# Optimization experiments

Measured on AMD Instinct MI355X. Metric: run time of the kernel, lower is better.

## Reference

```python
import jax, jax.numpy as jnp
import numpy as np

N = 100000   # nodes
E = 3200000  # edges (before self-loops)
H = 16       # hidden_dim
G = 1000     # graphs in batch
NEG_SLOPE = 0.2


def setup_inputs() -> dict:
    key = jax.random.key(0)
    ks = jax.random.split(key, 40)
    rn = lambda k, s: (jax.random.normal(k, s, jnp.float32) * 0.1)
    inp = {}
    inp['x'] = jax.random.normal(ks[0], (N, 1), jnp.float32)
    inp['edge_index'] = jax.random.randint(ks[1], (2, E), 0, N, jnp.int64)
    inp['batch'] = jnp.sort(jax.random.randint(ks[2], (N,), 0, G, jnp.int64))
    dims = [1, H, H]
    i = 3
    for l in range(3):
        d = dims[l]
        inp[f'c{l}_Wl'] = rn(ks[i], (d, H)); i += 1
        inp[f'c{l}_bl'] = jnp.zeros((H,), jnp.float32)
        inp[f'c{l}_Wr'] = rn(ks[i], (d, H)); i += 1
        inp[f'c{l}_br'] = jnp.zeros((H,), jnp.float32)
        inp[f'c{l}_att'] = rn(ks[i], (H,)); i += 1
        inp[f'c{l}_bias'] = jnp.zeros((H,), jnp.float32)
        inp[f'l{l}_W'] = rn(ks[i], (H, H)); i += 1
        inp[f'l{l}_b'] = jnp.zeros((H,), jnp.float32)
    for j, (a, b) in enumerate([(H, H), (H, H), (H, 1)]):
        inp[f'o{j}_W'] = rn(ks[i], (a, b)); i += 1
        inp[f'o{j}_b'] = jnp.zeros((b,), jnp.float32)
    return inp


def gatv2_conv(x, src, dst, Wl, bl, Wr, br, att, bias):
    # PyG GATv2Conv, heads=1: x_j = lin_l(x)[src], x_i = lin_r(x)[dst]
    xl = x @ Wl + bl  # [N,H] source transform
    xr = x @ Wr + br  # [N,H] target transform
    e = jax.nn.leaky_relu(xl[src] + xr[dst], NEG_SLOPE)  # [E+N,H]
    score = e @ att  # [E+N]
    # scatter-softmax over incoming edges of each destination node
    m = jax.ops.segment_max(score, dst, num_segments=N)
    ex = jnp.exp(score - m[dst])
    denom = jax.ops.segment_sum(ex, dst, num_segments=N)
    alpha = ex / denom[dst]
    out = jax.ops.segment_sum(alpha[:, None] * xl[src], dst, num_segments=N)
    return out + bias


def reference(x, c0_Wl, c0_bl, c0_Wr, c0_br, c0_att, c0_bias,
              c1_Wl, c1_bl, c1_Wr, c1_br, c1_att, c1_bias,
              c2_Wl, c2_bl, c2_Wr, c2_br, c2_att, c2_bias,
              l0_W, l0_b, l1_W, l1_b, l2_W, l2_b,
              o0_W, o0_b, o1_W, o1_b, o2_W, o2_b,
              edge_index, batch):
    # add self-loops (PyG GATv2Conv default add_self_loops=True)
    loops = jnp.arange(N, dtype=edge_index.dtype)
    ei = jnp.concatenate([edge_index, jnp.stack([loops, loops])], axis=1)
    src, dst = ei[0], ei[1]
    convs = [(c0_Wl, c0_bl, c0_Wr, c0_br, c0_att, c0_bias),
             (c1_Wl, c1_bl, c1_Wr, c1_br, c1_att, c1_bias),
             (c2_Wl, c2_bl, c2_Wr, c2_br, c2_att, c2_bias)]
    lins = [(l0_W, l0_b), (l1_W, l1_b), (l2_W, l2_b)]
    h = x
    for (Wl, bl, Wr, br, att, bias), (W, b) in zip(convs, lins):
        h = jax.nn.relu(gatv2_conv(h, src, dst, Wl, bl, Wr, br, att, bias))
        h = h @ W + b
    g = jax.ops.segment_sum(h, batch, num_segments=G)  # global_add_pool -> [G,H]
    g = jax.nn.relu(g @ o0_W + o0_b)
    g = jax.nn.relu(g @ o1_W + o1_b)
    return g @ o2_W + o2_b  # [G,1]
```

## Files before the change

### kernel.cpp

```cpp
#include <hip/hip_runtime.h>
#include <hip/hip_fp16.h>

#define HD 16

static constexpr int NN = 100000;
static constexpr int EE = 3200000;
static constexpr int GG = 1000;
static constexpr int ET = EE + NN;
static constexpr float NEG = 0.2f;
static constexpr float LOG2E = 1.44269504f;

static constexpr int BSH = 8;
static constexpr int NB = (NN + 255) >> BSH;
static constexpr int EPB = 8192;
static constexpr int GB = (ET + EPB - 1) / EPB;
static constexpr int ITER = EPB / 1024;

__device__ __forceinline__ int imin(int a, int b) { return a < b ? a : b; }

__device__ __forceinline__ float h2f(unsigned short u) {
  __half_raw r; r.x = u;
  return __half2float((__half)r);
}

__device__ __forceinline__ float quad_sum(float v) {
  int a = __builtin_amdgcn_update_dpp(0, __float_as_int(v), 0xB1, 0xF, 0xF, true);
  v += __int_as_float(a);
  int b = __builtin_amdgcn_update_dpp(0, __float_as_int(v), 0x4E, 0xF, 0xF, true);
  return v + __int_as_float(b);
}

__global__ void k_chist(const int* __restrict__ edst, int* __restrict__ chist) {
  __shared__ int sh[NB];
  int t = threadIdx.x;
  for (int i = t; i < NB; i += 1024) sh[i] = 0;
  __syncthreads();
  int b0 = blockIdx.x * EPB;
#pragma unroll
  for (int i = 0; i < ITER; ++i) {
    int e = b0 + t + i * 1024;
    if (e < ET) {
      int d = (e < EE) ? edst[e] : e - EE;
      atomicAdd(&sh[d >> BSH], 1);
    }
  }
  __syncthreads();
  for (int i = t; i < NB; i += 1024)
    if (sh[i]) atomicAdd(&chist[i], sh[i]);
}

__global__ void k_cscan(const int* __restrict__ chist, int* __restrict__ cbase,
                        int* __restrict__ ccur, int* __restrict__ rowptr) {
  __shared__ int sh[512];
  int t = threadIdx.x;
  sh[t] = (t < NB) ? chist[t] : 0;
  __syncthreads();
  for (int off = 1; off < 512; off <<= 1) {
    int v = sh[t];
    int a = (t >= off) ? sh[t - off] : 0;
    __syncthreads();
    sh[t] = v + a;
    __syncthreads();
  }
  if (t < NB) {
    int b = (t == 0) ? 0 : sh[t - 1];
    cbase[t] = b;
    ccur[t] = b;
  }
  if (t == 0) rowptr[NN] = ET;
}

__global__ void k_csplit(const int* __restrict__ esrc, const int* __restrict__ edst,
                         int* __restrict__ ccur, unsigned* __restrict__ tmp) {
  __shared__ int hist[NB];
  __shared__ int base[NB];
  int t = threadIdx.x;
  for (int i = t; i < NB; i += 1024) hist[i] = 0;
  __syncthreads();
  int b0 = blockIdx.x * EPB;
  int sl[ITER], dl[ITER];
#pragma unroll
  for (int i = 0; i < ITER; ++i) {
    int e = b0 + t + i * 1024;
    int s = -1, d = 0;
    if (e < ET) {
      if (e < EE) { s = esrc[e]; d = edst[e]; } else { s = e - EE; d = s; }
      atomicAdd(&hist[d >> BSH], 1);
    }
    sl[i] = s; dl[i] = d;
  }
  __syncthreads();
  for (int i = t; i < NB; i += 1024) {
    int c = hist[i];
    base[i] = c ? atomicAdd(&ccur[i], c) : 0;
    hist[i] = 0;
  }
  __syncthreads();
#pragma unroll
  for (int i = 0; i < ITER; ++i) {
    int s = sl[i];
    if (s >= 0) {
      int d = dl[i], bb = d >> BSH;
      int slot = base[bb] + atomicAdd(&hist[bb], 1);
      tmp[slot] = ((unsigned)(d & 255) << 17) | (unsigned)s;
    }
  }
}

__global__ void k_fsort(const unsigned* __restrict__ tmp, const int* __restrict__ cbase,
                        const int* __restrict__ chist, int* __restrict__ rowptr,
                        int* __restrict__ psrc) {
  __shared__ int fh[256];
  __shared__ int fs[256];
  int b = blockIdx.x, t = threadIdx.x;
  if (t < 256) fh[t] = 0;
  __syncthreads();
  int beg = cbase[b], cnt = chist[b];
  for (int i = t; i < cnt; i += 1024)
    atomicAdd(&fh[tmp[beg + i] >> 17], 1);
  __syncthreads();
  if (t < 256) fs[t] = fh[t];
  __syncthreads();
  for (int off = 1; off < 256; off <<= 1) {
    int v = 0, a = 0;
    if (t < 256) { v = fs[t]; if (t >= off) a = fs[t - off]; }
    __syncthreads();
    if (t < 256) fs[t] = v + a;
    __syncthreads();
  }
  if (t < 256) {
    int ex = fs[t] - fh[t];
    fs[t] = ex;
    int node = (b << BSH) + t;
    if (node < NN) rowptr[node] = beg + ex;
  }
  __syncthreads();
  for (int i = t; i < cnt; i += 1024) {
    unsigned v = tmp[beg + i];
    int ld = v >> 17;
    psrc[beg + atomicAdd(&fs[ld], 1)] = (int)(v & 0x1FFFFu);
  }
}

__global__ void k_comb(const float* __restrict__ W0, const float* __restrict__ b0,
                       const float* __restrict__ Wl1, const float* __restrict__ bl1,
                       const float* __restrict__ Wr1, const float* __restrict__ br1,
                       const float* __restrict__ W1, const float* __restrict__ b1,
                       const float* __restrict__ Wl2, const float* __restrict__ bl2,
                       const float* __restrict__ Wr2, const float* __restrict__ br2,
                       float* __restrict__ Wc0l, float* __restrict__ bc0l,
                       float* __restrict__ Wc0r, float* __restrict__ bc0r,
                       float* __restrict__ Wc1l, float* __restrict__ bc1l,
                       float* __restrict__ Wc1r, float* __restrict__ bc1r) {
  const float *W, *b, *P, *bp;
  float *Wo, *bo;
  switch (blockIdx.x) {
    case 0:  W = W0; b = b0; P = Wl1; bp = bl1; Wo = Wc0l; bo = bc0l; break;
    case 1:  W = W0; b = b0; P = Wr1; bp = br1; Wo = Wc0r; bo = bc0r; break;
    case 2:  W = W1; b = b1; P = Wl2; bp = bl2; Wo = Wc1l; bo = bc1l; break;
    default: W = W1; b = b1; P = Wr2; bp = br2; Wo = Wc1r; bo = bc1r; break;
  }
  int t = threadIdx.x;
  int c = t >> 4, k = t & 15;
  float s = 0.f;
#pragma unroll
  for (int i = 0; i < 16; ++i) s = fmaf(W[c * 16 + i], P[i * 16 + k], s);
  Wo[t] = s;
  if (t < 16) {
    float sb = bp[t];
#pragma unroll
    for (int i = 0; i < 16; ++i) sb = fmaf(b[i], P[i * 16 + t], sb);
    bo[t] = sb;
  }
}

template <int MODE>
__global__ void k_conv(const int* __restrict__ rowptr, const int* __restrict__ psrc,
                       const float* __restrict__ x,
                       const float* __restrict__ Wl0, const float* __restrict__ bl0,
                       const float* __restrict__ Wr0, const float* __restrict__ br0,
                       const __half* __restrict__ xlh, const float* __restrict__ xr,
                       const float* __restrict__ att, const float* __restrict__ cbias,
                       const float* __restrict__ Wcl, const float* __restrict__ bcl,
                       const float* __restrict__ Wcr, const float* __restrict__ bcr,
                       const float* __restrict__ Wlast, const float* __restrict__ blast,
                       __half* __restrict__ oxlh, float* __restrict__ oxr,
                       float* __restrict__ gpool, const int* __restrict__ batch) {
  __shared__ float hsh[4][16];
  int gt = blockIdx.x * blockDim.x + threadIdx.x;
  int n = gt >> 6;
  if (n >= NN) return;
  int lane = threadIdx.x & 63;
  int q = lane & 3;
  int ei = lane >> 2;
  int k0 = q * 4;
  float4 att4 = *reinterpret_cast<const float4*>(att + k0);
  att4.x *= LOG2E; att4.y *= LOG2E; att4.z *= LOG2E; att4.w *= LOG2E;
  float4 xr4, wl4, bl4;
  if constexpr (MODE == 0) {
    wl4 = *reinterpret_cast<const float4*>(Wl0 + k0);
    bl4 = *reinterpret_cast<const float4*>(bl0 + k0);
    float4 wr4 = *reinterpret_cast<const float4*>(Wr0 + k0);
    float4 br4 = *reinterpret_cast<const float4*>(br0 + k0);
    float xn = x[n];
    xr4.x = fmaf(xn, wr4.x, br4.x);
    xr4.y = fmaf(xn, wr4.y, br4.y);
    xr4.z = fmaf(xn, wr4.z, br4.z);
    xr4.w = fmaf(xn, wr4.w, br4.w);
  } else {
    xr4 = *reinterpret_cast<const float4*>(xr + (size_t)n * HD + k0);
  }
  int beg = rowptr[n], end = rowptr[n + 1];
  int e1 = end - 1;
  int p = beg + ei;
  int s0 = psrc[imin(p, e1)];
  int s1 = psrc[imin(p + 16, e1)];
  float l0 = 0.f, l1 = 0.f;
  float a00 = 0.f, a01 = 0.f, a02 = 0.f, a03 = 0.f;
  float a10 = 0.f, a11 = 0.f, a12 = 0.f, a13 = 0.f;
  for (; p < end; p += 32) {
    int t0 = psrc[imin(p + 32, e1)];
    int t1 = psrc[imin(p + 48, e1)];
    float x00, x01, x02, x03, x10, x11, x12, x13;
    if constexpr (MODE == 0) {
      float xs0 = x[s0], xs1 = x[s1];
      x00 = fmaf(xs0, wl4.x, bl4.x); x01 = fmaf(xs0, wl4.y, bl4.y);
      x02 = fmaf(xs0, wl4.z, bl4.z); x03 = fmaf(xs0, wl4.w, bl4.w);
      x10 = fmaf(xs1, wl4.x, bl4.x); x11 = fmaf(xs1, wl4.y, bl4.y);
      x12 = fmaf(xs1, wl4.z, bl4.z); x13 = fmaf(xs1, wl4.w, bl4.w);
    } else {
      ushort4 r0 = *reinterpret_cast<const ushort4*>(xlh + (size_t)s0 * HD + k0);
      ushort4 r1 = *reinterpret_cast<const ushort4*>(xlh + (size_t)s1 * HD + k0);
      x00 = h2f(r0.x); x01 = h2f(r0.y); x02 = h2f(r0.z); x03 = h2f(r0.w);
      x10 = h2f(r1.x); x11 = h2f(r1.y); x12 = h2f(r1.z); x13 = h2f(r1.w);
    }
    float u, sp0 = 0.f, sp1 = 0.f;
    u = x00 + xr4.x; u = fmaxf(u, NEG * u); sp0 = fmaf(u, att4.x, sp0);
    u = x01 + xr4.y; u = fmaxf(u, NEG * u); sp0 = fmaf(u, att4.y, sp0);
    u = x02 + xr4.z; u = fmaxf(u, NEG * u); sp0 = fmaf(u, att4.z, sp0);
    u = x03 + xr4.w; u = fmaxf(u, NEG * u); sp0 = fmaf(u, att4.w, sp0);
    u = x10 + xr4.x; u = fmaxf(u, NEG * u); sp1 = fmaf(u, att4.x, sp1);
    u = x11 + xr4.y; u = fmaxf(u, NEG * u); sp1 = fmaf(u, att4.y, sp1);
    u = x12 + xr4.z; u = fmaxf(u, NEG * u); sp1 = fmaf(u, att4.z, sp1);
    u = x13 + xr4.w; u = fmaxf(u, NEG * u); sp1 = fmaf(u, att4.w, sp1);
    float sc0 = quad_sum(sp0);
    float sc1 = quad_sum(sp1);
    float pe0 = __builtin_amdgcn_exp2f(sc0);
    float pe1 = (p + 16 < end) ? __builtin_amdgcn_exp2f(sc1) : 0.f;
    l0 += pe0;
    a00 = fmaf(pe0, x00, a00); a01 = fmaf(pe0, x01, a01);
    a02 = fmaf(pe0, x02, a02); a03 = fmaf(pe0, x03, a03);
    l1 += pe1;
    a10 = fmaf(pe1, x10, a10); a11 = fmaf(pe1, x11, a11);
    a12 = fmaf(pe1, x12, a12); a13 = fmaf(pe1, x13, a13);
    s0 = t0; s1 = t1;
  }
  float l = l0 + l1;
  float b0 = a00 + a10, b1 = a01 + a11, b2 = a02 + a12, b3 = a03 + a13;
#pragma unroll
  for (int st = 4; st <= 32; st <<= 1) {
    l += __shfl_xor(l, st, 64);
    b0 += __shfl_xor(b0, st, 64);
    b1 += __shfl_xor(b1, st, 64);
    b2 += __shfl_xor(b2, st, 64);
    b3 += __shfl_xor(b3, st, 64);
  }
  float rl = __builtin_amdgcn_rcpf(l);
  float4 cb4 = *reinterpret_cast<const float4*>(cbias + k0);
  float h0 = fmaxf(fmaf(b0, rl, cb4.x), 0.f);
  float h1 = fmaxf(fmaf(b1, rl, cb4.y), 0.f);
  float h2 = fmaxf(fmaf(b2, rl, cb4.z), 0.f);
  float h3 = fmaxf(fmaf(b3, rl, cb4.w), 0.f);
  int w = threadIdx.x >> 6;
  if (lane < 4)
    *reinterpret_cast<float4*>(&hsh[w][lane * 4]) = make_float4(h0, h1, h2, h3);
  int sub = lane >> 4;
  int k = lane & 15;
  float hk = hsh[w][k];
  if constexpr (MODE == 2) {
    float o = 0.f;
#pragma unroll
    for (int i = 0; i < 4; ++i) {
      int c = 4 * sub + i;
      float hc = __shfl(hk, c, 16);
      o = fmaf(hc, Wlast[c * HD + k], o);
    }
    o += __shfl_xor(o, 16, 64);
    o += __shfl_xor(o, 32, 64);
    if (sub == 0) atomicAdd(gpool + (size_t)batch[n] * HD + k, o + blast[k]);
  } else {
    const float* Wsel = (sub < 2) ? Wcl : Wcr;
    int cb = (sub & 1) * 8;
    float o = 0.f;
#pragma unroll
    for (int i = 0; i < 8; ++i) {
      int c = cb + i;
      float hc = __shfl(hk, c, 16);
      o = fmaf(hc, Wsel[c * HD + k], o);
    }
    o += __shfl_xor(o, 16, 64);
    if (sub == 0) oxlh[(size_t)n * HD + k] = __float2half(o + bcl[k]);
    else if (sub == 2) oxr[(size_t)n * HD + k] = o + bcr[k];
  }
}

__global__ void k_mlp(const float* __restrict__ g,
                      const float* __restrict__ W0, const float* __restrict__ b0,
                      const float* __restrict__ W1, const float* __restrict__ b1,
                      const float* __restrict__ W2, const float* __restrict__ b2,
                      float* __restrict__ out) {
  int gi = blockIdx.x * blockDim.x + threadIdx.x;
  if (gi >= GG) return;
  float v[HD], a[HD];
  const float4* g4 = reinterpret_cast<const float4*>(g + (size_t)gi * HD);
#pragma unroll
  for (int i = 0; i < 4; ++i) {
    float4 tv = g4[i];
    v[4 * i] = tv.x; v[4 * i + 1] = tv.y; v[4 * i + 2] = tv.z; v[4 * i + 3] = tv.w;
  }
#pragma unroll
  for (int j = 0; j < HD; ++j) {
    float s = b0[j];
#pragma unroll
    for (int kk = 0; kk < HD; ++kk) s = fmaf(v[kk], W0[kk * HD + j], s);
    a[j] = s > 0.f ? s : 0.f;
  }
#pragma unroll
  for (int j = 0; j < HD; ++j) {
    float s = b1[j];
#pragma unroll
    for (int kk = 0; kk < HD; ++kk) s = fmaf(a[kk], W1[kk * HD + j], s);
    v[j] = s > 0.f ? s : 0.f;
  }
  float s = b2[0];
#pragma unroll
  for (int kk = 0; kk < HD; ++kk) s = fmaf(v[kk], W2[kk], s);
  out[gi] = s;
}

extern "C" void kernel_launch(void* const* d_in, const int* in_sizes, int n_in,
                              void* d_out, int out_size, void* d_ws, size_t ws_size,
                              hipStream_t stream) {
  const float* x = (const float*)d_in[0];
  const int* ei = (const int*)d_in[1];
  const int* batch = (const int*)d_in[2];
  const int* esrc = ei;
  const int* edst = ei + EE;

  const float* cW[3][6];
  const float* lW[3][2];
  int i = 3;
  for (int l = 0; l < 3; ++l) {
    for (int j = 0; j < 6; ++j) cW[l][j] = (const float*)d_in[i++];
    lW[l][0] = (const float*)d_in[i++];
    lW[l][1] = (const float*)d_in[i++];
  }
  const float *oW[3], *ob[3];
  for (int j = 0; j < 3; ++j) {
    oW[j] = (const float*)d_in[i++];
    ob[j] = (const float*)d_in[i++];
  }

  char* ws = (char*)d_ws;
  size_t off = 0;
  auto alloc = [&](size_t bytes) {
    void* p = ws + off;
    off = (off + bytes + 255) & ~(size_t)255;
    return p;
  };
  int* psrc = (int*)alloc((size_t)ET * 4);
  int* rowptr = (int*)alloc((size_t)(NN + 1) * 4);
  int* chist = (int*)alloc((size_t)NB * 4);
  int* cbase = (int*)alloc((size_t)NB * 4);
  int* ccur = (int*)alloc((size_t)NB * 4);
  float* Wc0l = (float*)alloc(256 * 4);
  float* Wc0r = (float*)alloc(256 * 4);
  float* Wc1l = (float*)alloc(256 * 4);
  float* Wc1r = (float*)alloc(256 * 4);
  float* bc0l = (float*)alloc(16 * 4);
  float* bc0r = (float*)alloc(16 * 4);
  float* bc1l = (float*)alloc(16 * 4);
  float* bc1r = (float*)alloc(16 * 4);
  size_t NNHD = (size_t)NN * HD;
  size_t featBytes = NNHD * 12 + (size_t)GG * HD * 4;
  size_t uniBytes = (size_t)ET * 4 > featBytes ? (size_t)ET * 4 : featBytes;
  char* uni = (char*)alloc(uniBytes);
  unsigned* tmp = (unsigned*)uni;
  __half* xlhB = (__half*)uni;
  float* xrB = (float*)(uni + NNHD * 2);
  __half* xlhA = (__half*)(uni + NNHD * 6);
  float* xrA = (float*)(uni + NNHD * 8);
  float* gbuf = (float*)(uni + NNHD * 12);

  const int B = 256;
  const int gConv = (NN * 64 + B - 1) / B;
  const int gMlp = (GG + B - 1) / B;

  hipMemsetAsync(chist, 0, (size_t)NB * 4, stream);

  k_comb<<<4, 256, 0, stream>>>(lW[0][0], lW[0][1],
                                cW[1][0], cW[1][1], cW[1][2], cW[1][3],
                                lW[1][0], lW[1][1],
                                cW[2][0], cW[2][1], cW[2][2], cW[2][3],
                                Wc0l, bc0l, Wc0r, bc0r, Wc1l, bc1l, Wc1r, bc1r);

  k_chist<<<GB, 1024, 0, stream>>>(edst, chist);
  k_cscan<<<1, 512, 0, stream>>>(chist, cbase, ccur, rowptr);
  k_csplit<<<GB, 1024, 0, stream>>>(esrc, edst, ccur, tmp);
  k_fsort<<<NB, 1024, 0, stream>>>(tmp, cbase, chist, rowptr, psrc);

  hipMemsetAsync(gbuf, 0, (size_t)GG * HD * 4, stream);

  k_conv<0><<<gConv, B, 0, stream>>>(rowptr, psrc, x,
                                     cW[0][0], cW[0][1], cW[0][2], cW[0][3],
                                     nullptr, nullptr, cW[0][4], cW[0][5],
                                     Wc0l, bc0l, Wc0r, bc0r, nullptr, nullptr,
                                     xlhB, xrB, nullptr, nullptr);
  k_conv<1><<<gConv, B, 0, stream>>>(rowptr, psrc, nullptr,
                                     nullptr, nullptr, nullptr, nullptr,
                                     xlhB, xrB, cW[1][4], cW[1][5],
                                     Wc1l, bc1l, Wc1r, bc1r, nullptr, nullptr,
                                     xlhA, xrA, nullptr, nullptr);
  k_conv<2><<<gConv, B, 0, stream>>>(rowptr, psrc, nullptr,
                                     nullptr, nullptr, nullptr, nullptr,
                                     xlhA, xrA, cW[2][4], cW[2][5],
                                     nullptr, nullptr, nullptr, nullptr,
                                     lW[2][0], lW[2][1],
                                     nullptr, nullptr, gbuf, batch);

  k_mlp<<<gMlp, B, 0, stream>>>(gbuf, oW[0], ob[0], oW[1], ob[1], oW[2], ob[2],
                                (float*)d_out);
}
```

Before: 245.7 us.

## Process two destination nodes per wavefront in GATv2 conv kernel

Splits each 64-lane wavefront into two 32-lane halves, each handling its own destination node, so the grid is halved and waves spend less time on idle lanes for nodes with around 33 incoming edges. The cross-lane reductions move from xor shuffles to DPP row-rotate adds plus one shuffle, and the trailing linear layer reads hidden values straight from shared memory instead of broadcasting them with shuffles. Each half-wave now walks its edge list in steps of 16 rather than 32, so high-degree nodes take more serial iterations. Each lane also does more multiply-adds per output in the epilogue.

```diff
diff --git a/kernel.cpp b/kernel.cpp
--- a/kernel.cpp
+++ b/kernel.cpp
@@ -23,11 +23,21 @@
   return __half2float((__half)r);
 }
 
+template <int N>
+__device__ __forceinline__ float row_ror_add(float v) {
+  int m = __builtin_amdgcn_update_dpp(0, __float_as_int(v), 0x120 + N, 0xF, 0xF, true);
+  return v + __int_as_float(m);
+}
 __device__ __forceinline__ float quad_sum(float v) {
   int a = __builtin_amdgcn_update_dpp(0, __float_as_int(v), 0xB1, 0xF, 0xF, true);
   v += __int_as_float(a);
   int b = __builtin_amdgcn_update_dpp(0, __float_as_int(v), 0x4E, 0xF, 0xF, true);
   return v + __int_as_float(b);
+}
+__device__ __forceinline__ float slot_sum16(float v) {
+  v = row_ror_add<4>(v);
+  v = row_ror_add<8>(v);
+  return v;
 }
 
 __global__ void k_chist(const int* __restrict__ edst, int* __restrict__ chist) {
@@ -186,13 +196,16 @@
                        const float* __restrict__ Wlast, const float* __restrict__ blast,
                        __half* __restrict__ oxlh, float* __restrict__ oxr,
                        float* __restrict__ gpool, const int* __restrict__ batch) {
-  __shared__ float hsh[4][16];
+  __shared__ float hsh[4][2][16];
   int gt = blockIdx.x * blockDim.x + threadIdx.x;
-  int n = gt >> 6;
+  int wave = gt >> 6;
+  int lane = threadIdx.x & 63;
+  int hf = lane >> 5;
+  int lane5 = lane & 31;
+  int ei = lane5 >> 2;
+  int q = lane & 3;
+  int n = wave * 2 + hf;
   if (n >= NN) return;
-  int lane = threadIdx.x & 63;
-  int q = lane & 3;
-  int ei = lane >> 2;
   int k0 = q * 4;
   float4 att4 = *reinterpret_cast<const float4*>(att + k0);
   att4.x *= LOG2E; att4.y *= LOG2E; att4.z *= LOG2E; att4.w *= LOG2E;
@@ -214,13 +227,13 @@
   int e1 = end - 1;
   int p = beg + ei;
   int s0 = psrc[imin(p, e1)];
-  int s1 = psrc[imin(p + 16, e1)];
+  int s1 = psrc[imin(p + 8, e1)];
   float l0 = 0.f, l1 = 0.f;
   float a00 = 0.f, a01 = 0.f, a02 = 0.f, a03 = 0.f;
   float a10 = 0.f, a11 = 0.f, a12 = 0.f, a13 = 0.f;
-  for (; p < end; p += 32) {
-    int t0 = psrc[imin(p + 32, e1)];
-    int t1 = psrc[imin(p + 48, e1)];
+  for (; p < end; p += 16) {
+    int t0 = psrc[imin(p + 16, e1)];
+    int t1 = psrc[imin(p + 24, e1)];
     float x00, x01, x02, x03, x10, x11, x12, x13;
     if constexpr (MODE == 0) {
       float xs0 = x[s0], xs1 = x[s1];
@@ -246,7 +259,7 @@
     float sc0 = quad_sum(sp0);
     float sc1 = quad_sum(sp1);
     float pe0 = __builtin_amdgcn_exp2f(sc0);
-    float pe1 = (p + 16 < end) ? __builtin_amdgcn_exp2f(sc1) : 0.f;
+    float pe1 = (p + 8 < end) ? __builtin_amdgcn_exp2f(sc1) : 0.f;
     l0 += pe0;
     a00 = fmaf(pe0, x00, a00); a01 = fmaf(pe0, x01, a01);
     a02 = fmaf(pe0, x02, a02); a03 = fmaf(pe0, x03, a03);
@@ -257,14 +270,14 @@
   }
   float l = l0 + l1;
   float b0 = a00 + a10, b1 = a01 + a11, b2 = a02 + a12, b3 = a03 + a13;
-#pragma unroll
-  for (int st = 4; st <= 32; st <<= 1) {
-    l += __shfl_xor(l, st, 64);
-    b0 += __shfl_xor(b0, st, 64);
-    b1 += __shfl_xor(b1, st, 64);
-    b2 += __shfl_xor(b2, st, 64);
-    b3 += __shfl_xor(b3, st, 64);
-  }
+  l = slot_sum16(l);
+  b0 = slot_sum16(b0); b1 = slot_sum16(b1);
+  b2 = slot_sum16(b2); b3 = slot_sum16(b3);
+  l += __shfl_xor(l, 16, 64);
+  b0 += __shfl_xor(b0, 16, 64);
+  b1 += __shfl_xor(b1, 16, 64);
+  b2 += __shfl_xor(b2, 16, 64);
+  b3 += __shfl_xor(b3, 16, 64);
   float rl = __builtin_amdgcn_rcpf(l);
   float4 cb4 = *reinterpret_cast<const float4*>(cbias + k0);
   float h0 = fmaxf(fmaf(b0, rl, cb4.x), 0.f);
@@ -272,35 +285,27 @@
   float h2 = fmaxf(fmaf(b2, rl, cb4.z), 0.f);
   float h3 = fmaxf(fmaf(b3, rl, cb4.w), 0.f);
   int w = threadIdx.x >> 6;
-  if (lane < 4)
-    *reinterpret_cast<float4*>(&hsh[w][lane * 4]) = make_float4(h0, h1, h2, h3);
-  int sub = lane >> 4;
-  int k = lane & 15;
-  float hk = hsh[w][k];
+  if (lane5 < 4)
+    *reinterpret_cast<float4*>(&hsh[w][hf][lane5 * 4]) = make_float4(h0, h1, h2, h3);
+  int sub = lane5 >> 4;
+  int k = lane5 & 15;
+  const float* hrow = hsh[w][hf];
   if constexpr (MODE == 2) {
     float o = 0.f;
 #pragma unroll
-    for (int i = 0; i < 4; ++i) {
-      int c = 4 * sub + i;
-      float hc = __shfl(hk, c, 16);
-      o = fmaf(hc, Wlast[c * HD + k], o);
+    for (int i = 0; i < 8; ++i) {
+      int c = 8 * sub + i;
+      o = fmaf(hrow[c], Wlast[c * HD + k], o);
     }
     o += __shfl_xor(o, 16, 64);
-    o += __shfl_xor(o, 32, 64);
     if (sub == 0) atomicAdd(gpool + (size_t)batch[n] * HD + k, o + blast[k]);
   } else {
-    const float* Wsel = (sub < 2) ? Wcl : Wcr;
-    int cb = (sub & 1) * 8;
+    const float* Wsel = sub ? Wcr : Wcl;
     float o = 0.f;
 #pragma unroll
-    for (int i = 0; i < 8; ++i) {
-      int c = cb + i;
-      float hc = __shfl(hk, c, 16);
-      o = fmaf(hc, Wsel[c * HD + k], o);
-    }
-    o += __shfl_xor(o, 16, 64);
+    for (int c = 0; c < 16; ++c) o = fmaf(hrow[c], Wsel[c * HD + k], o);
     if (sub == 0) oxlh[(size_t)n * HD + k] = __float2half(o + bcl[k]);
-    else if (sub == 2) oxr[(size_t)n * HD + k] = o + bcr[k];
+    else          oxr[(size_t)n * HD + k] = o + bcr[k];
   }
 }
 
@@ -393,7 +398,7 @@
   float* gbuf = (float*)(uni + NNHD * 12);
 
   const int B = 256;
-  const int gConv = (NN * 64 + B - 1) / B;
+  const int gConv = (NN * 32 + B - 1) / B;
   const int gMlp = (GG + B - 1) / B;
 
   hipMemsetAsync(chist, 0, (size_t)NB * 4, stream);
```

Result: faster. 209.1 us (-14.9%).
